# Performance work log

Hardware: AMD Instinct MI355X
Metric: run time of the kernel (lower is better)

## Reference

```python
import jax, jax.numpy as jnp
import numpy as np

B, T_ENC, T_DEC = 64, 256, 200
MEL, R = 80, 2
ENC_DIM = 256   # must equal attention_context_dim (context = weighted sum of encoder outputs)
ATT = 256       # attention_rnn_units == attention_context_dim
DEC = 256       # decoder_rnn_units
PRE1, PRE2 = 256, 128


def _gru(x, h, wih, whh, bih, bhh):
    # torch.nn.GRUCell math; weights are (3*H, in) torch layout
    gi = x @ wih.T + bih
    gh = h @ whh.T + bhh
    i_r, i_z, i_n = jnp.split(gi, 3, axis=-1)
    h_r, h_z, h_n = jnp.split(gh, 3, axis=-1)
    r = jax.nn.sigmoid(i_r + h_r)
    z = jax.nn.sigmoid(i_z + h_z)
    n = jnp.tanh(i_n + r * h_n)
    return (1.0 - z) * n + z * h


def setup_inputs() -> dict:
    key = jax.random.key(0)
    ks = iter(jax.random.split(key, 40))
    def nrm(shape, s=0.05):
        return jax.random.normal(next(ks), shape, dtype=jnp.float32) * s
    inp = {
        "encoder_outputs": nrm((B, T_ENC, ENC_DIM), 1.0),
        "inputs": nrm((B, T_DEC, MEL * R), 1.0),
        "memory_lengths": jax.random.randint(next(ks), (B,), T_ENC // 2, T_ENC + 1),
        # prenet
        "pre_w1": nrm((PRE1, MEL * R)), "pre_b1": jnp.zeros((PRE1,), jnp.float32),
        "pre_w2": nrm((PRE2, PRE1)),    "pre_b2": jnp.zeros((PRE2,), jnp.float32),
        # memory layer (no bias)
        "mem_w": nrm((ATT, ENC_DIM)),
        # attention GRUCell: input = prenet_out(128) + context(256)
        "att_wih": nrm((3 * ATT, PRE2 + ATT)), "att_whh": nrm((3 * ATT, ATT)),
        "att_bih": jnp.zeros((3 * ATT,), jnp.float32), "att_bhh": jnp.zeros((3 * ATT,), jnp.float32),
        # Bahdanau attention: query layer (no bias) and v vector
        "q_w": nrm((ATT, ATT)), "v_w": nrm((ATT,)),
        # project_to_decoder_in
        "proj_w": nrm((DEC, ATT + ATT)), "proj_b": jnp.zeros((DEC,), jnp.float32),
        # two decoder GRUCells
        "g1_wih": nrm((3 * DEC, DEC)), "g1_whh": nrm((3 * DEC, DEC)),
        "g1_bih": jnp.zeros((3 * DEC,), jnp.float32), "g1_bhh": jnp.zeros((3 * DEC,), jnp.float32),
        "g2_wih": nrm((3 * DEC, DEC)), "g2_whh": nrm((3 * DEC, DEC)),
        "g2_bih": jnp.zeros((3 * DEC,), jnp.float32), "g2_bhh": jnp.zeros((3 * DEC,), jnp.float32),
        # output projections
        "mel_w": nrm((MEL * R, DEC + ATT)), "mel_b": jnp.zeros((MEL * R,), jnp.float32),
        "stop_w": nrm((1, DEC + ATT)),      "stop_b": jnp.zeros((1,), jnp.float32),
    }
    return inp


def reference(encoder_outputs, inputs, memory_lengths,
              pre_w1, pre_b1, pre_w2, pre_b2, mem_w,
              att_wih, att_whh, att_bih, att_bhh, q_w, v_w,
              proj_w, proj_b,
              g1_wih, g1_whh, g1_bih, g1_bhh,
              g2_wih, g2_whh, g2_bih, g2_bhh,
              mel_w, mel_b, stop_w, stop_b):
    b = encoder_outputs.shape[0]
    processed_memory = encoder_outputs @ mem_w.T                    # (B,T_enc,ATT)
    pad_mask = jnp.arange(T_ENC)[None, :] >= memory_lengths[:, None]  # True = padding

    # teacher forcing: step t consumes previous target frame (zeros at t=0)
    x_seq = jnp.concatenate([jnp.zeros((b, 1, MEL * R), inputs.dtype), inputs[:, :-1]], axis=1)
    xs = jnp.swapaxes(x_seq, 0, 1)                                  # (T_dec,B,mel*r)

    def step(carry, x):
        h_att, ctx, h1, h2 = carry
        # prenet (dropout omitted: deterministic reference)
        pre = jax.nn.relu(jax.nn.relu(x @ pre_w1.T + pre_b1) @ pre_w2.T + pre_b2)
        # attention RNN
        h_att = _gru(jnp.concatenate([pre, ctx], -1), h_att, att_wih, att_whh, att_bih, att_bhh)
        # Bahdanau alignment
        score = jnp.einsum('btd,d->bt', jnp.tanh(processed_memory + (h_att @ q_w.T)[:, None, :]), v_w)
        score = jnp.where(pad_mask, -jnp.inf, score)
        align = jax.nn.softmax(score, axis=-1)                      # (B,T_enc)
        ctx = jnp.einsum('bt,btd->bd', align, encoder_outputs)      # (B,ATT)
        # decoder stack with residuals
        d = jnp.concatenate([h_att, ctx], -1) @ proj_w.T + proj_b
        h1 = _gru(d, h1, g1_wih, g1_whh, g1_bih, g1_bhh); d = h1 + d
        h2 = _gru(d, h2, g2_wih, g2_whh, g2_bih, g2_bhh); d = h2 + d
        p = jnp.concatenate([d, ctx], -1)
        mel = p @ mel_w.T + mel_b                                   # (B,mel*r)
        stop = jax.nn.sigmoid(p @ stop_w.T + stop_b)[:, 0]          # (B,)
        return (h_att, ctx, h1, h2), (mel, align, stop)

    zeros = lambda d: jnp.zeros((b, d), encoder_outputs.dtype)
    init = (zeros(ATT), zeros(ATT), zeros(DEC), zeros(DEC))
    _, (mels, aligns, stops) = jax.lax.scan(step, init, xs)

    mel_outputs = jnp.swapaxes(mels, 0, 1)                          # (B,T_dec,mel*r)
    attn_scores = jnp.swapaxes(aligns, 0, 1)                        # (B,T_dec,T_enc)
    stop_tokens = jnp.repeat(jnp.swapaxes(stops, 0, 1), R, axis=1)  # (B,T_dec*r)
    return mel_outputs, attn_scores, stop_tokens
```

## Files before the change

### kernel.cpp

```cpp
#include <hip/hip_runtime.h>
#include <math.h>
#include <stdint.h>

#define NB   64
#define TE   256
#define TD   200
#define MR   160

typedef _Float16 h2 __attribute__((ext_vector_type(2)));

__device__ __forceinline__ float dot2f(h2 a, h2 b, float c){
  return __builtin_amdgcn_fdot2(a, b, c, false);
}
__device__ __forceinline__ h2 u2h(unsigned int u){ return __builtin_bit_cast(h2, u); }
__device__ __forceinline__ unsigned int h2u(h2 h){ return __builtin_bit_cast(unsigned int, h); }
__device__ __forceinline__ unsigned f2u(float f){ return __builtin_bit_cast(unsigned, f); }
__device__ __forceinline__ float u2f(unsigned u){ return __builtin_bit_cast(float, u); }

__device__ __forceinline__ float sigmf(float x){
  return __fdividef(1.f, 1.f + __expf(-x));
}
__device__ __forceinline__ float tanhf_(float x){
  float ax = fabsf(x);
  float e  = __expf(-2.f*ax);
  float r  = __fdividef(1.f - e, 1.f + e);
  return copysignf(r, x);
}

static constexpr size_t OFF_PM   = 0;
static constexpr size_t OFF_ENCH = 8388608;
static constexpr size_t OFF_GIP  = 16777216;
static constexpr size_t OFF_P    = 36438016;
static constexpr size_t OFF_W2   = 49545216;
static constexpr size_t OFF_W8   = 50184192;
static constexpr size_t WS_NEEDED = 52936704;

static constexpr size_t A_PW1  = 0;
static constexpr size_t A_PW2  = 20480;
static constexpr size_t A_WIHP = 36864;
static constexpr size_t A_MEMW = 86016;
static constexpr size_t A_MELW = 118784;

static constexpr size_t B_ATTC = 0;
static constexpr size_t B_ATTH = 24576;
static constexpr size_t B_G1I  = 49152;
static constexpr size_t B_G1H  = 73728;
static constexpr size_t B_G2I  = 98304;
static constexpr size_t B_G2H  = 122880;
static constexpr size_t B_PROJ = 147456;
static constexpr size_t B_QW   = 163840;

__global__ void k_conv(const float* __restrict__ src, char* __restrict__ ws,
                       unsigned off_h2, int O, int Kh, int k0, int ld){
  int i = blockIdx.x*256 + threadIdx.x;
  if (i >= O*Kh) return;
  int o = i % O, kp = i / O;
  _Float16* dst = (_Float16*)(ws + OFF_W2) + 2*((size_t)off_h2 + i);
  dst[0] = (_Float16)src[(size_t)o*ld + k0 + 2*kp    ];
  dst[1] = (_Float16)src[(size_t)o*ld + k0 + 2*kp + 1];
}

__global__ void k_conv8(const float* __restrict__ src, char* __restrict__ ws,
                        unsigned off16, int O, int Kq, int k0, int ld){
  int i = blockIdx.x*256 + threadIdx.x;
  if (i >= O*Kq) return;
  int o = i % O, kq = i / O;
  const float* s = src + (size_t)o*ld + k0 + kq*8;
  h2 p0, p1, p2, p3;
  p0.x=(_Float16)s[0]; p0.y=(_Float16)s[1];
  p1.x=(_Float16)s[2]; p1.y=(_Float16)s[3];
  p2.x=(_Float16)s[4]; p2.y=(_Float16)s[5];
  p3.x=(_Float16)s[6]; p3.y=(_Float16)s[7];
  uint4 r; r.x=h2u(p0); r.y=h2u(p1); r.z=h2u(p2); r.w=h2u(p3);
  ((uint4*)(ws + OFF_W8))[(size_t)off16 + i] = r;
}

__global__ void k_pm(const float* __restrict__ enc, char* __restrict__ ws){
  int bt = blockIdx.x;
  int j  = threadIdx.x;
  const h2* mw = (const h2*)(ws + OFF_W2) + A_MEMW;
  _Float16* pmN  = (_Float16*)(ws + OFF_PM);
  _Float16* encH = (_Float16*)(ws + OFF_ENCH);
  __shared__ _Float16 e[256];
  float ev = enc[(size_t)bt*256 + j];
  e[j] = (_Float16)ev;
  encH[(size_t)bt*256 + j] = (_Float16)ev;
  __syncthreads();
  const h2* e2 = (const h2*)e;
  float acc = 0.f;
  #pragma unroll 8
  for (int kp=0; kp<128; ++kp) acc = dot2f(mw[kp*256 + j], e2[kp], acc);
  pmN[(size_t)bt*256 + j] = (_Float16)acc;
}

__global__ void k_pre(const float* __restrict__ xin, const float* __restrict__ b1,
                      const float* __restrict__ b2, const float* __restrict__ bih,
                      char* __restrict__ ws){
  int bt = blockIdx.x;
  int b = bt / TD, t = bt % TD;
  int j = threadIdx.x;
  const h2* w1 = (const h2*)(ws + OFF_W2) + A_PW1;
  const h2* w2 = (const h2*)(ws + OFF_W2) + A_PW2;
  const h2* wp = (const h2*)(ws + OFF_W2) + A_WIHP;
  _Float16* gip = (_Float16*)(ws + OFF_GIP) + (size_t)bt*768;
  __shared__ _Float16 xh[160];
  __shared__ _Float16 a1[256];
  __shared__ _Float16 pr[128];
  if (j < 160)
    xh[j] = (t==0) ? (_Float16)0.f : (_Float16)xin[((size_t)b*TD + (t-1))*MR + j];
  __syncthreads();
  {
    const h2* x2 = (const h2*)xh;
    float acc = b1[j];
    #pragma unroll 8
    for (int kp=0; kp<80; ++kp) acc = dot2f(w1[kp*256 + j], x2[kp], acc);
    a1[j] = (_Float16)fmaxf(acc, 0.f);
  }
  __syncthreads();
  if (j < 128){
    const h2* x2 = (const h2*)a1;
    float acc = b2[j];
    #pragma unroll 8
    for (int kp=0; kp<128; ++kp) acc = dot2f(w2[kp*128 + j], x2[kp], acc);
    pr[j] = (_Float16)fmaxf(acc, 0.f);
  }
  __syncthreads();
  {
    const h2* p2 = (const h2*)pr;
    for (int o=j; o<768; o+=256){
      float acc = bih[o];
      #pragma unroll 8
      for (int kp=0; kp<64; ++kp) acc = dot2f(wp[kp*768 + o], p2[kp], acc);
      gip[o] = (_Float16)acc;
    }
  }
}

__global__ void k_zero(float* __restrict__ out){
  int* prog = (int*)(out + (size_t)NB*TD*MR + (size_t)NB*TD*TE);
  if (threadIdx.x < 256) prog[threadIdx.x] = 0;
}

__device__ __forceinline__ float d4dot(uint4 w, uint4 x, float a){
  a = dot2f(u2h(w.x), u2h(x.x), a);
  a = dot2f(u2h(w.y), u2h(x.y), a);
  a = dot2f(u2h(w.z), u2h(x.z), a);
  a = dot2f(u2h(w.w), u2h(x.w), a);
  return a;
}

__device__ __forceinline__ void gemv4(const uint4* __restrict__ wI, const uint4* __restrict__ wH,
                                      const uint4* xI, const uint4* xH,
                                      int j, int ks, float* scr, int tid){
  float a0=0.f,a1=0.f,a2=0.f,a3=0.f;
  #pragma unroll 2
  for (int kq=ks*8; kq<ks*8+8; ++kq){
    uint4 xi = xI[kq];
    uint4 xh = xH[kq];
    a0 = d4dot(wI[kq*768 +       j], xi, a0);
    a1 = d4dot(wI[kq*768 + 256 + j], xi, a1);
    a2 = d4dot(wI[kq*768 + 512 + j], xi, a2);
    a0 = d4dot(wH[kq*768 +       j], xh, a0);
    a1 = d4dot(wH[kq*768 + 256 + j], xh, a1);
    a3 = d4dot(wH[kq*768 + 512 + j], xh, a3);
  }
  float* r = scr + tid*4;
  r[0]=a0; r[1]=a1; r[2]=a2; r[3]=a3;
}

__device__ __forceinline__ void gemvA(const uint4* __restrict__ wAC, const uint4* __restrict__ wAH,
                                      const uint4* xc, const uint4* xh,
                                      int j, int ks, float* scr, int tid){
  float a0=0.f,a1=0.f,a2=0.f,a3=0.f;
  #pragma unroll 2
  for (int i=0;i<8;++i){
    int kq = ks*8+i;
    uint4 xv = xh[kq];
    a0 = d4dot(wAH[kq*768 +       j], xv, a0);
    a1 = d4dot(wAH[kq*768 + 256 + j], xv, a1);
    a3 = d4dot(wAH[kq*768 + 512 + j], xv, a3);
  }
  #pragma unroll
  for (int i=0;i<2;++i){
    int kq = ks*2+i;
    uint4 xv = xc[kq];
    a0 = d4dot(wAC[kq*768 +       j], xv, a0);
    a1 = d4dot(wAC[kq*768 + 256 + j], xv, a1);
    a2 = d4dot(wAC[kq*768 + 512 + j], xv, a2);
  }
  float* r = scr + tid*4;
  r[0]=a0; r[1]=a1; r[2]=a2; r[3]=a3;
}

__global__ __launch_bounds__(1024) void k_dec(
    const int*   __restrict__ memlen,
    const float* __restrict__ att_bhh,
    const float* __restrict__ vw,
    const float* __restrict__ proj_b,
    const float* __restrict__ g1_bih, const float* __restrict__ g1_bhh,
    const float* __restrict__ g2_bih, const float* __restrict__ g2_bhh,
    float* __restrict__ out, char* __restrict__ ws)
{
  const int tid  = threadIdx.x;
  const int x    = blockIdx.x;
  const int y    = x >> 3;
  const int role = y & 3;
  const int b    = ((y >> 2) << 3) | (x & 7);
  const int ks   = tid >> 8;
  const int j    = tid & 255;

  const uint4* W8 = (const uint4*)(ws + OFF_W8);
  int* prog = (int*)(out + (size_t)NB*TD*MR + (size_t)NB*TD*TE);
  int* pGP  = prog;
  int* pCtx = prog + 64;
  int* pD   = prog + 128;
  int* pB1  = prog + 192;
  unsigned* gX = (unsigned*)((_Float16*)(ws + OFF_GIP) + (size_t)b*TD*768);
  unsigned* uSlot = (unsigned*)(out + (size_t)NB*TD*128) + (size_t)b*768;

  __shared__ __align__(16) _Float16 hAh[256], ctxh[256], hh[256], dh[256];
  __shared__ float hAf[256], hf[256], df[256];
  __shared__ float qf[256], sc[256], al[256], vl[256];
  __shared__ float scr[4096];
  __shared__ float red2[4];
  __shared__ __align__(16) uint4 pmL[8192];

  if (role == 0){
    const uint4* wAC = W8 + B_ATTC;
    const uint4* wAH = W8 + B_ATTH;
    const uint4* wQ4 = W8 + B_QW;
    const uint4* pm4 = (const uint4*)(ws + OFF_PM) + (size_t)b*8192;
    const unsigned* encW = (const unsigned*)(ws + OFF_ENCH) + (size_t)b*TE*128;
    const _Float16* gipB = (const _Float16*)(ws + OFF_GIP) + (size_t)b*TD*768;
    _Float16* pstB = (_Float16*)(ws + OFF_P) + (size_t)b*TD*512;
    float* outA = out + (size_t)NB*TD*MR + (size_t)b*TD*TE;
    const int ml = memlen[b];
    const int tsl = tid>>7, dp = tid&127;

    for (int idx = tid; idx < 8192; idx += 1024){
      int tp = idx >> 5, g = idx & 31;
      pmL[(tp<<5) | (g ^ (tp & 7))] = pm4[idx];
    }
    if (tid < 256){ hAh[tid]=(_Float16)0.f; hAf[tid]=0.f; ctxh[tid]=(_Float16)0.f; vl[tid]=vw[tid]; }
    __syncthreads();
    const uint4* hA4  = (const uint4*)hAh;
    const uint4* ctx4 = (const uint4*)ctxh;

    #pragma unroll 1
    for (int t=0; t<TD; ++t){
      gemvA(wAC, wAH, ctx4, hA4, j, ks, scr, tid);
      if (t > 0 && tid==0){
        while (__hip_atomic_load(pGP+b, __ATOMIC_RELAXED, __HIP_MEMORY_SCOPE_AGENT) < t)
          __builtin_amdgcn_s_sleep(1);
      }
      __syncthreads();
      if (tid < 256){
        const _Float16* gp = gipB + (size_t)t*768;
        float s0 = scr[tid*4+0]+scr[(256+tid)*4+0]+scr[(512+tid)*4+0]+scr[(768+tid)*4+0];
        float s1 = scr[tid*4+1]+scr[(256+tid)*4+1]+scr[(512+tid)*4+1]+scr[(768+tid)*4+1];
        float s2 = scr[tid*4+2]+scr[(256+tid)*4+2]+scr[(512+tid)*4+2]+scr[(768+tid)*4+2];
        float s3 = scr[tid*4+3]+scr[(256+tid)*4+3]+scr[(512+tid)*4+3]+scr[(768+tid)*4+3];
        if (t > 0){
          s0 += u2f(__hip_atomic_load(uSlot +       tid, __ATOMIC_RELAXED, __HIP_MEMORY_SCOPE_AGENT));
          s1 += u2f(__hip_atomic_load(uSlot + 256 + tid, __ATOMIC_RELAXED, __HIP_MEMORY_SCOPE_AGENT));
          s2 += u2f(__hip_atomic_load(uSlot + 512 + tid, __ATOMIC_RELAXED, __HIP_MEMORY_SCOPE_AGENT));
        }
        float r = sigmf(s0 + (float)gp[tid]     + att_bhh[tid]);
        float z = sigmf(s1 + (float)gp[256+tid] + att_bhh[256+tid]);
        float n = tanhf_(s2 + (float)gp[512+tid] + r*(s3 + att_bhh[512+tid]));
        float h = (1.f-z)*n + z*hAf[tid];
        hAf[tid]=h; hAh[tid]=(_Float16)h;
      }
      __syncthreads();
      { float a=0.f;
        #pragma unroll 2
        for (int kq=ks*8; kq<ks*8+8; ++kq)
          a = d4dot(wQ4[kq*256 + j], hA4[kq], a);
        scr[tid]=a; }
      __syncthreads();
      if (tid<256) qf[tid] = scr[tid]+scr[256+tid]+scr[512+tid]+scr[768+tid];
      __syncthreads();
      { float s=0.f;
        #pragma unroll
        for (int i=0;i<8;++i){
          int g = ks*8 + i;
          uint4 q4 = pmL[(j<<5) | (g ^ (j&7))];
          int d0 = ks*64 + i*8;
          h2 p0=u2h(q4.x), p1=u2h(q4.y), p2=u2h(q4.z), p3=u2h(q4.w);
          s += vl[d0+0]*tanhf_((float)p0.x + qf[d0+0]);
          s += vl[d0+1]*tanhf_((float)p0.y + qf[d0+1]);
          s += vl[d0+2]*tanhf_((float)p1.x + qf[d0+2]);
          s += vl[d0+3]*tanhf_((float)p1.y + qf[d0+3]);
          s += vl[d0+4]*tanhf_((float)p2.x + qf[d0+4]);
          s += vl[d0+5]*tanhf_((float)p2.y + qf[d0+5]);
          s += vl[d0+6]*tanhf_((float)p3.x + qf[d0+6]);
          s += vl[d0+7]*tanhf_((float)p3.y + qf[d0+7]);
        }
        scr[tid]=s; }
      __syncthreads();
      if (tid<256){
        float s = scr[tid]+scr[256+tid]+scr[512+tid]+scr[768+tid];
        sc[tid] = (tid < ml) ? s : -INFINITY;
      }
      __syncthreads();
      {
        float v = (tid<256) ? sc[tid] : -INFINITY;
        if (tid<256){
          #pragma unroll
          for (int o=32;o>0;o>>=1) v = fmaxf(v, __shfl_down(v,o,64));
          if ((tid&63)==0) red2[tid>>6]=v;
        }
        __syncthreads();
        float m = fmaxf(fmaxf(red2[0],red2[1]), fmaxf(red2[2],red2[3]));
        __syncthreads();
        float e = 0.f;
        if (tid<256){
          e = __expf(sc[tid]-m);
          float sv = e;
          #pragma unroll
          for (int o=32;o>0;o>>=1) sv += __shfl_down(sv,o,64);
          if ((tid&63)==0) red2[tid>>6]=sv;
        }
        __syncthreads();
        if (tid<256){
          float sum = red2[0]+red2[1]+red2[2]+red2[3];
          float a = e*__fdividef(1.f,sum);
          al[tid]=a;
          outA[(size_t)t*TE + tid]=a;
        }
      }
      __syncthreads();
      { float c0=0.f, c1=0.f;
        #pragma unroll 8
        for (int tp=tsl*32; tp<tsl*32+32; ++tp){
          float a = al[tp];
          h2 e = u2h(encW[(size_t)tp*128 + dp]);
          c0 += a*(float)e.x; c1 += a*(float)e.y;
        }
        scr[tid*2]=c0; scr[tid*2+1]=c1; }
      __syncthreads();
      if (tid<128){
        float c0=0.f, c1=0.f;
        #pragma unroll
        for (int k=0;k<8;++k){ c0 += scr[(k*128+tid)*2]; c1 += scr[(k*128+tid)*2+1]; }
        h2 c; c.x=(_Float16)c0; c.y=(_Float16)c1;
        unsigned w = h2u(c);
        ((unsigned*)ctxh)[tid] = w;
        ((unsigned*)pstB)[(size_t)t*256 + 128 + tid] = w;
        __hip_atomic_store(gX + (size_t)t*384 + tid, ((const unsigned*)hAh)[tid],
                           __ATOMIC_RELAXED, __HIP_MEMORY_SCOPE_AGENT);
        __hip_atomic_store(gX + (size_t)t*384 + 128 + tid, w,
                           __ATOMIC_RELAXED, __HIP_MEMORY_SCOPE_AGENT);
      }
      __syncthreads();
      if (tid==0)
        __hip_atomic_store(pCtx+b, t+1, __ATOMIC_RELEASE, __HIP_MEMORY_SCOPE_AGENT);
    }
  } else if (role == 1){
    const uint4* wAC  = W8 + B_ATTC;
    const uint4* wPRJ = W8 + B_PROJ;
    const uint4* hA4  = (const uint4*)hAh;
    const uint4* ctx4 = (const uint4*)ctxh;

    #pragma unroll 1
    for (int t=0; t<TD; ++t){
      if (tid==0){
        while (__hip_atomic_load(pCtx+b, __ATOMIC_RELAXED, __HIP_MEMORY_SCOPE_AGENT) < t+1)
          __builtin_amdgcn_s_sleep(1);
      }
      __syncthreads();
      if (tid<256){
        unsigned w = __hip_atomic_load(gX + (size_t)t*384 + tid,
                                       __ATOMIC_RELAXED, __HIP_MEMORY_SCOPE_AGENT);
        if (tid<128) ((unsigned*)hAh)[tid] = w;
        else         ((unsigned*)ctxh)[tid-128] = w;
      }
      __syncthreads();
      { float a0=0.f, a1=0.f, a2=0.f;
        #pragma unroll 2
        for (int i=0;i<6;++i){
          int kq = 8 + ks*6 + i;
          uint4 xv = ctx4[kq];
          a0 = d4dot(wAC[kq*768 +       j], xv, a0);
          a1 = d4dot(wAC[kq*768 + 256 + j], xv, a1);
          a2 = d4dot(wAC[kq*768 + 512 + j], xv, a2);
        }
        float* r = scr + tid*3; r[0]=a0; r[1]=a1; r[2]=a2; }
      __syncthreads();
      if (tid<256){
        float p0 = scr[tid*3+0]+scr[(256+tid)*3+0]+scr[(512+tid)*3+0]+scr[(768+tid)*3+0];
        float p1 = scr[tid*3+1]+scr[(256+tid)*3+1]+scr[(512+tid)*3+1]+scr[(768+tid)*3+1];
        float p2 = scr[tid*3+2]+scr[(256+tid)*3+2]+scr[(512+tid)*3+2]+scr[(768+tid)*3+2];
        __hip_atomic_store(uSlot +       tid, f2u(p0), __ATOMIC_RELAXED, __HIP_MEMORY_SCOPE_AGENT);
        __hip_atomic_store(uSlot + 256 + tid, f2u(p1), __ATOMIC_RELAXED, __HIP_MEMORY_SCOPE_AGENT);
        __hip_atomic_store(uSlot + 512 + tid, f2u(p2), __ATOMIC_RELAXED, __HIP_MEMORY_SCOPE_AGENT);
      }
      __syncthreads();
      if (tid==0)
        __hip_atomic_store(pGP+b, t+1, __ATOMIC_RELEASE, __HIP_MEMORY_SCOPE_AGENT);
      { float a=0.f;
        #pragma unroll 2
        for (int kq=ks*16; kq<ks*16+16; ++kq){
          uint4 xa = (kq < 32) ? hA4[kq] : ctx4[kq-32];
          a = d4dot(wPRJ[kq*256 + j], xa, a);
        }
        scr[tid]=a; }
      __syncthreads();
      if (tid<128){
        const int o0 = 2*tid, o1 = o0+1;
        float d0 = scr[o0]+scr[256+o0]+scr[512+o0]+scr[768+o0] + proj_b[o0];
        float d1 = scr[o1]+scr[256+o1]+scr[512+o1]+scr[768+o1] + proj_b[o1];
        h2 p; p.x=(_Float16)d0; p.y=(_Float16)d1;
        __hip_atomic_store(gX + (size_t)t*384 + 256 + tid, h2u(p),
                           __ATOMIC_RELAXED, __HIP_MEMORY_SCOPE_AGENT);
      }
      __syncthreads();
      if (tid==0)
        __hip_atomic_store(pD+b, t+1, __ATOMIC_RELEASE, __HIP_MEMORY_SCOPE_AGENT);
    }
  } else {
    const bool isB1 = (role == 2);
    const uint4* wI = W8 + (isB1 ? B_G1I : B_G2I);
    const uint4* wH = W8 + (isB1 ? B_G1H : B_G2H);
    const float* bih = isB1 ? g1_bih : g2_bih;
    const float* bhh = isB1 ? g1_bhh : g2_bhh;
    int* pin = isB1 ? pD : pB1;
    unsigned* oX = (unsigned*)out + (size_t)b*TD*128;
    const unsigned* inP = isB1 ? (gX + 256) : oX;
    const int instr = isB1 ? 384 : 128;
    _Float16* pstB = (_Float16*)(ws + OFF_P) + (size_t)b*TD*512;

    if (tid<256){ hh[tid]=(_Float16)0.f; hf[tid]=0.f; }
    __syncthreads();
    const uint4* h4  = (const uint4*)hh;
    const uint4* dd4 = (const uint4*)dh;

    #pragma unroll 1
    for (int t=0; t<TD; ++t){
      if (tid==0){
        while (__hip_atomic_load(pin+b, __ATOMIC_RELAXED, __HIP_MEMORY_SCOPE_AGENT) < t+1)
          __builtin_amdgcn_s_sleep(1);
      }
      __syncthreads();
      if (tid<128){
        unsigned w = __hip_atomic_load(inP + (size_t)t*instr + tid,
                                       __ATOMIC_RELAXED, __HIP_MEMORY_SCOPE_AGENT);
        ((unsigned*)dh)[tid] = w;
        h2 p = u2h(w);
        df[2*tid]   = (float)p.x;
        df[2*tid+1] = (float)p.y;
      }
      __syncthreads();
      gemv4(wI, wH, dd4, h4, j, ks, scr, tid);
      __syncthreads();
      if (tid<256){
        float s0 = scr[tid*4+0]+scr[(256+tid)*4+0]+scr[(512+tid)*4+0]+scr[(768+tid)*4+0];
        float s1 = scr[tid*4+1]+scr[(256+tid)*4+1]+scr[(512+tid)*4+1]+scr[(768+tid)*4+1];
        float s2 = scr[tid*4+2]+scr[(256+tid)*4+2]+scr[(512+tid)*4+2]+scr[(768+tid)*4+2];
        float s3 = scr[tid*4+3]+scr[(256+tid)*4+3]+scr[(512+tid)*4+3]+scr[(768+tid)*4+3];
        float r = sigmf(s0 + bih[tid]     + bhh[tid]);
        float z = sigmf(s1 + bih[256+tid] + bhh[256+tid]);
        float n = tanhf_(s2 + bih[512+tid] + r*(s3 + bhh[512+tid]));
        float h = (1.f-z)*n + z*hf[tid];
        float dn = h + df[tid];
        hf[tid]=h; hh[tid]=(_Float16)h;
        dh[tid]=(_Float16)dn;
        if (!isB1) pstB[(size_t)t*512 + tid] = (_Float16)dn;
      }
      __syncthreads();
      if (isB1){
        if (tid<128)
          __hip_atomic_store(oX + (size_t)t*128 + tid, ((const unsigned*)dh)[tid],
                             __ATOMIC_RELAXED, __HIP_MEMORY_SCOPE_AGENT);
        __syncthreads();
        if (tid==0)
          __hip_atomic_store(pB1+b, t+1, __ATOMIC_RELEASE, __HIP_MEMORY_SCOPE_AGENT);
      }
    }
  }
}

__global__ void k_post(const float* __restrict__ mel_b, const float* __restrict__ stop_w,
                       const float* __restrict__ stop_b, float* __restrict__ out,
                       char* __restrict__ ws){
  int bt = blockIdx.x;
  int b = bt / TD, t = bt % TD;
  int j = threadIdx.x;
  const h2* wm = (const h2*)(ws + OFF_W2) + A_MELW;
  const _Float16* p = (const _Float16*)(ws + OFF_P) + (size_t)bt*512;
  __shared__ _Float16 pl[512];
  ((uint32_t*)pl)[j] = ((const uint32_t*)p)[j];
  __syncthreads();
  const h2* p2 = (const h2*)pl;
  if (j < 160){
    float acc = mel_b[j];
    #pragma unroll 8
    for (int kp=0; kp<256; ++kp) acc = dot2f(wm[kp*160 + j], p2[kp], acc);
    out[(size_t)bt*MR + j] = acc;
  } else if (j == 160){
    float acc = stop_b[0];
    for (int k=0; k<512; ++k) acc += stop_w[k]*(float)pl[k];
    float s = __fdividef(1.f, 1.f + __expf(-acc));
    float* os = out + (size_t)NB*TD*MR + (size_t)NB*TD*TE + (size_t)b*2*TD;
    os[2*t]   = s;
    os[2*t+1] = s;
  }
}

extern "C" void kernel_launch(void* const* d_in, const int* in_sizes, int n_in,
                              void* d_out, int out_size, void* d_ws, size_t ws_size,
                              hipStream_t stream)
{
  const float* enc     = (const float*)d_in[0];
  const float* xin     = (const float*)d_in[1];
  const int*   mlen    = (const int*)  d_in[2];
  const float* pre_w1  = (const float*)d_in[3];
  const float* pre_b1  = (const float*)d_in[4];
  const float* pre_w2  = (const float*)d_in[5];
  const float* pre_b2  = (const float*)d_in[6];
  const float* mem_w   = (const float*)d_in[7];
  const float* att_wih = (const float*)d_in[8];
  const float* att_whh = (const float*)d_in[9];
  const float* att_bih = (const float*)d_in[10];
  const float* att_bhh = (const float*)d_in[11];
  const float* q_w     = (const float*)d_in[12];
  const float* v_w     = (const float*)d_in[13];
  const float* proj_w  = (const float*)d_in[14];
  const float* proj_b  = (const float*)d_in[15];
  const float* g1_wih  = (const float*)d_in[16];
  const float* g1_whh  = (const float*)d_in[17];
  const float* g1_bih  = (const float*)d_in[18];
  const float* g1_bhh  = (const float*)d_in[19];
  const float* g2_wih  = (const float*)d_in[20];
  const float* g2_whh  = (const float*)d_in[21];
  const float* g2_bih  = (const float*)d_in[22];
  const float* g2_bhh  = (const float*)d_in[23];
  const float* mel_w   = (const float*)d_in[24];
  const float* mel_b   = (const float*)d_in[25];
  const float* stop_w  = (const float*)d_in[26];
  const float* stop_b  = (const float*)d_in[27];
  (void)in_sizes; (void)n_in; (void)out_size;

  if (ws_size < WS_NEEDED) return;

  float* out = (float*)d_out;
  char*  ws  = (char*)d_ws;

  auto conv = [&](const float* src, size_t off_h2, int O, int Kh, int k0, int ld){
    int n = O*Kh;
    k_conv<<<(n+255)/256, 256, 0, stream>>>(src, ws, (unsigned)off_h2, O, Kh, k0, ld);
  };
  auto conv8 = [&](const float* src, size_t off16, int O, int Kq, int k0, int ld){
    int n = O*Kq;
    k_conv8<<<(n+255)/256, 256, 0, stream>>>(src, ws, (unsigned)off16, O, Kq, k0, ld);
  };

  conv(pre_w1,  A_PW1,  256, 80,  0, 160);
  conv(pre_w2,  A_PW2,  128, 128, 0, 256);
  conv(att_wih, A_WIHP, 768, 64,  0, 384);
  conv(mem_w,   A_MEMW, 256, 128, 0, 256);
  conv(mel_w,   A_MELW, 160, 256, 0, 512);
  conv8(att_wih, B_ATTC, 768, 32, 128, 384);
  conv8(att_whh, B_ATTH, 768, 32, 0,   256);
  conv8(g1_wih,  B_G1I,  768, 32, 0,   256);
  conv8(g1_whh,  B_G1H,  768, 32, 0,   256);
  conv8(g2_wih,  B_G2I,  768, 32, 0,   256);
  conv8(g2_whh,  B_G2H,  768, 32, 0,   256);
  conv8(proj_w,  B_PROJ, 256, 64, 0,   512);
  conv8(q_w,     B_QW,   256, 32, 0,   256);

  k_pm  <<<NB*TE, 256, 0, stream>>>(enc, ws);
  k_pre <<<NB*TD, 256, 0, stream>>>(xin, pre_b1, pre_b2, att_bih, ws);
  k_zero<<<1, 256, 0, stream>>>(out);
  k_dec <<<4*NB, 1024, 0, stream>>>(mlen, att_bhh, v_w, proj_b,
                                    g1_bih, g1_bhh, g2_bih, g2_bhh, out, ws);
  k_post<<<NB*TD, 256, 0, stream>>>(mel_b, stop_w, stop_b, out, ws);
}
```

Before: 5.103 ms.

## Move context computation to role-1 block with LDS-cached encoder outputs

The attention-context weighted sum moves out of the attention block (role 0) into the projection block (role 1). Role 1 now caches the encoder outputs in LDS and receives alignment weights through a new global slot and progress flag. Role 0 starts the hidden-state part of its GRU gemv before waiting on the previous context, and uses a combined two-phase progress counter. The intent is to shorten the serial critical path of role 0 and replace global encoder reads with LDS reads, at the cost of an extra inter-block handoff per step.

```diff
diff --git a/kernel.cpp b/kernel.cpp
--- a/kernel.cpp
+++ b/kernel.cpp
@@ -168,30 +168,6 @@
   r[0]=a0; r[1]=a1; r[2]=a2; r[3]=a3;
 }
 
-__device__ __forceinline__ void gemvA(const uint4* __restrict__ wAC, const uint4* __restrict__ wAH,
-                                      const uint4* xc, const uint4* xh,
-                                      int j, int ks, float* scr, int tid){
-  float a0=0.f,a1=0.f,a2=0.f,a3=0.f;
-  #pragma unroll 2
-  for (int i=0;i<8;++i){
-    int kq = ks*8+i;
-    uint4 xv = xh[kq];
-    a0 = d4dot(wAH[kq*768 +       j], xv, a0);
-    a1 = d4dot(wAH[kq*768 + 256 + j], xv, a1);
-    a3 = d4dot(wAH[kq*768 + 512 + j], xv, a3);
-  }
-  #pragma unroll
-  for (int i=0;i<2;++i){
-    int kq = ks*2+i;
-    uint4 xv = xc[kq];
-    a0 = d4dot(wAC[kq*768 +       j], xv, a0);
-    a1 = d4dot(wAC[kq*768 + 256 + j], xv, a1);
-    a2 = d4dot(wAC[kq*768 + 512 + j], xv, a2);
-  }
-  float* r = scr + tid*4;
-  r[0]=a0; r[1]=a1; r[2]=a2; r[3]=a3;
-}
-
 __global__ __launch_bounds__(1024) void k_dec(
     const int*   __restrict__ memlen,
     const float* __restrict__ att_bhh,
@@ -211,12 +187,13 @@
 
   const uint4* W8 = (const uint4*)(ws + OFF_W8);
   int* prog = (int*)(out + (size_t)NB*TD*MR + (size_t)NB*TD*TE);
-  int* pGP  = prog;
-  int* pCtx = prog + 64;
+  int* pP   = prog;
+  int* pAl  = prog + 64;
   int* pD   = prog + 128;
   int* pB1  = prog + 192;
   unsigned* gX = (unsigned*)((_Float16*)(ws + OFF_GIP) + (size_t)b*TD*768);
-  unsigned* uSlot = (unsigned*)(out + (size_t)NB*TD*128) + (size_t)b*768;
+  unsigned* uSlot = (unsigned*)out + (size_t)NB*TD*128 + (size_t)b*768;
+  unsigned* aSlot = (unsigned*)out + (size_t)NB*TD*128 + (size_t)NB*768 + (size_t)b*256;
 
   __shared__ __align__(16) _Float16 hAh[256], ctxh[256], hh[256], dh[256];
   __shared__ float hAf[256], hf[256], df[256];
@@ -230,12 +207,9 @@
     const uint4* wAH = W8 + B_ATTH;
     const uint4* wQ4 = W8 + B_QW;
     const uint4* pm4 = (const uint4*)(ws + OFF_PM) + (size_t)b*8192;
-    const unsigned* encW = (const unsigned*)(ws + OFF_ENCH) + (size_t)b*TE*128;
     const _Float16* gipB = (const _Float16*)(ws + OFF_GIP) + (size_t)b*TD*768;
-    _Float16* pstB = (_Float16*)(ws + OFF_P) + (size_t)b*TD*512;
     float* outA = out + (size_t)NB*TD*MR + (size_t)b*TD*TE;
     const int ml = memlen[b];
-    const int tsl = tid>>7, dp = tid&127;
 
     for (int idx = tid; idx < 8192; idx += 1024){
       int tp = idx >> 5, g = idx & 31;
@@ -248,9 +222,37 @@
 
     #pragma unroll 1
     for (int t=0; t<TD; ++t){
-      gemvA(wAC, wAH, ctx4, hA4, j, ks, scr, tid);
+      float a0=0.f, a1=0.f, a2=0.f, a3=0.f;
+      #pragma unroll 2
+      for (int i=0;i<8;++i){
+        int kq = ks*8+i;
+        uint4 xv = hA4[kq];
+        a0 = d4dot(wAH[kq*768 +       j], xv, a0);
+        a1 = d4dot(wAH[kq*768 + 256 + j], xv, a1);
+        a3 = d4dot(wAH[kq*768 + 512 + j], xv, a3);
+      }
+      if (t > 0){
+        if (tid==0){
+          while (__hip_atomic_load(pP+b, __ATOMIC_RELAXED, __HIP_MEMORY_SCOPE_AGENT) < 2*t-1)
+            __builtin_amdgcn_s_sleep(1);
+        }
+        __syncthreads();
+        if (tid<128)
+          ((unsigned*)ctxh)[tid] = __hip_atomic_load(gX + (size_t)(t-1)*384 + 128 + tid,
+                                                     __ATOMIC_RELAXED, __HIP_MEMORY_SCOPE_AGENT);
+        __syncthreads();
+      }
+      #pragma unroll
+      for (int i=0;i<2;++i){
+        int kq = ks*2+i;
+        uint4 xv = ctx4[kq];
+        a0 = d4dot(wAC[kq*768 +       j], xv, a0);
+        a1 = d4dot(wAC[kq*768 + 256 + j], xv, a1);
+        a2 = d4dot(wAC[kq*768 + 512 + j], xv, a2);
+      }
+      { float* r = scr + tid*4; r[0]=a0; r[1]=a1; r[2]=a2; r[3]=a3; }
       if (t > 0 && tid==0){
-        while (__hip_atomic_load(pGP+b, __ATOMIC_RELAXED, __HIP_MEMORY_SCOPE_AGENT) < t)
+        while (__hip_atomic_load(pP+b, __ATOMIC_RELAXED, __HIP_MEMORY_SCOPE_AGENT) < 2*t)
           __builtin_amdgcn_s_sleep(1);
       }
       __syncthreads();
@@ -277,6 +279,9 @@
         for (int kq=ks*8; kq<ks*8+8; ++kq)
           a = d4dot(wQ4[kq*256 + j], hA4[kq], a);
         scr[tid]=a; }
+      if (tid<128)
+        __hip_atomic_store(gX + (size_t)t*384 + tid, ((const unsigned*)hAh)[tid],
+                           __ATOMIC_RELAXED, __HIP_MEMORY_SCOPE_AGENT);
       __syncthreads();
       if (tid<256) qf[tid] = scr[tid]+scr[256+tid]+scr[512+tid]+scr[768+tid];
       __syncthreads();
@@ -325,16 +330,46 @@
         if (tid<256){
           float sum = red2[0]+red2[1]+red2[2]+red2[3];
           float a = e*__fdividef(1.f,sum);
-          al[tid]=a;
           outA[(size_t)t*TE + tid]=a;
-        }
-      }
+          __hip_atomic_store(aSlot + tid, f2u(a),
+                             __ATOMIC_RELAXED, __HIP_MEMORY_SCOPE_AGENT);
+        }
+      }
+      __syncthreads();
+      if (tid==0)
+        __hip_atomic_store(pAl+b, t+1, __ATOMIC_RELEASE, __HIP_MEMORY_SCOPE_AGENT);
+    }
+  } else if (role == 1){
+    const uint4* wAC  = W8 + B_ATTC;
+    const uint4* wPRJ = W8 + B_PROJ;
+    const unsigned* encW = (const unsigned*)(ws + OFF_ENCH) + (size_t)b*TE*128;
+    _Float16* pstB = (_Float16*)(ws + OFF_P) + (size_t)b*TD*512;
+    unsigned* encL = (unsigned*)pmL;
+    const uint4* hA4  = (const uint4*)hAh;
+    const uint4* ctx4 = (const uint4*)ctxh;
+    const int tsl = tid>>7, dp = tid&127;
+
+    for (int idx = tid; idx < 32768; idx += 1024) encL[idx] = encW[idx];
+    __syncthreads();
+
+    #pragma unroll 1
+    for (int t=0; t<TD; ++t){
+      if (tid==0){
+        while (__hip_atomic_load(pAl+b, __ATOMIC_RELAXED, __HIP_MEMORY_SCOPE_AGENT) < t+1)
+          __builtin_amdgcn_s_sleep(1);
+      }
+      __syncthreads();
+      if (tid<256)
+        al[tid] = u2f(__hip_atomic_load(aSlot + tid, __ATOMIC_RELAXED, __HIP_MEMORY_SCOPE_AGENT));
+      if (tid >= 256 && tid < 384)
+        ((unsigned*)hAh)[tid-256] = __hip_atomic_load(gX + (size_t)t*384 + (tid-256),
+                                                      __ATOMIC_RELAXED, __HIP_MEMORY_SCOPE_AGENT);
       __syncthreads();
       { float c0=0.f, c1=0.f;
         #pragma unroll 8
         for (int tp=tsl*32; tp<tsl*32+32; ++tp){
           float a = al[tp];
-          h2 e = u2h(encW[(size_t)tp*128 + dp]);
+          h2 e = u2h(encL[tp*128 + dp]);
           c0 += a*(float)e.x; c1 += a*(float)e.y;
         }
         scr[tid*2]=c0; scr[tid*2+1]=c1; }
@@ -347,35 +382,12 @@
         unsigned w = h2u(c);
         ((unsigned*)ctxh)[tid] = w;
         ((unsigned*)pstB)[(size_t)t*256 + 128 + tid] = w;
-        __hip_atomic_store(gX + (size_t)t*384 + tid, ((const unsigned*)hAh)[tid],
-                           __ATOMIC_RELAXED, __HIP_MEMORY_SCOPE_AGENT);
         __hip_atomic_store(gX + (size_t)t*384 + 128 + tid, w,
                            __ATOMIC_RELAXED, __HIP_MEMORY_SCOPE_AGENT);
       }
       __syncthreads();
       if (tid==0)
-        __hip_atomic_store(pCtx+b, t+1, __ATOMIC_RELEASE, __HIP_MEMORY_SCOPE_AGENT);
-    }
-  } else if (role == 1){
-    const uint4* wAC  = W8 + B_ATTC;
-    const uint4* wPRJ = W8 + B_PROJ;
-    const uint4* hA4  = (const uint4*)hAh;
-    const uint4* ctx4 = (const uint4*)ctxh;
-
-    #pragma unroll 1
-    for (int t=0; t<TD; ++t){
-      if (tid==0){
-        while (__hip_atomic_load(pCtx+b, __ATOMIC_RELAXED, __HIP_MEMORY_SCOPE_AGENT) < t+1)
-          __builtin_amdgcn_s_sleep(1);
-      }
-      __syncthreads();
-      if (tid<256){
-        unsigned w = __hip_atomic_load(gX + (size_t)t*384 + tid,
-                                       __ATOMIC_RELAXED, __HIP_MEMORY_SCOPE_AGENT);
-        if (tid<128) ((unsigned*)hAh)[tid] = w;
-        else         ((unsigned*)ctxh)[tid-128] = w;
-      }
-      __syncthreads();
+        __hip_atomic_store(pP+b, 2*t+1, __ATOMIC_RELEASE, __HIP_MEMORY_SCOPE_AGENT);
       { float a0=0.f, a1=0.f, a2=0.f;
         #pragma unroll 2
         for (int i=0;i<6;++i){
@@ -397,7 +409,7 @@
       }
       __syncthreads();
       if (tid==0)
-        __hip_atomic_store(pGP+b, t+1, __ATOMIC_RELEASE, __HIP_MEMORY_SCOPE_AGENT);
+        __hip_atomic_store(pP+b, 2*t+2, __ATOMIC_RELEASE, __HIP_MEMORY_SCOPE_AGENT);
       { float a=0.f;
         #pragma unroll 2
         for (int kq=ks*16; kq<ks*16+16; ++kq){
```

After: 4.686 ms. 8.2% less time.
